# Optimization experiments

Measured on AMD Instinct MI355X. Metric: run time of the kernel, lower is better.

## Reference

```python
import jax, jax.numpy as jnp
import numpy as np

B = 128; NMAX = 128; H = 1024; HH = 256; NZ = 64; M = 20; LAT = 128; NCLS = 10; SD = 5
IN_DIM = SD + NCLS + LAT  # 143


def setup_inputs() -> dict:
    key = jax.random.key(0)
    ks = jax.random.split(key, 24)
    r = lambda i, shape, s=0.05: jax.random.normal(ks[i], shape, dtype=jnp.float32) * s
    cls_idx = jax.random.randint(ks[20], (B,), 0, NCLS)
    return dict(
        z=jax.random.normal(ks[0], (B, LAT), dtype=jnp.float32),
        classifier=jax.nn.one_hot(cls_idx, NCLS, dtype=jnp.float32),
        fc_in_W=r(1, (2 * H + 2 * HH, LAT)),
        fc_in_b=jnp.zeros((2 * H + 2 * HH,), jnp.float32),
        Wx=r(2, (4 * H, IN_DIM)),
        Wh=r(3, (4 * H, H)),
        b0=jnp.zeros((4, H), jnp.float32),
        hWx=r(4, (4 * HH, IN_DIM + H)),
        hWh=r(5, (4 * HH, HH)),
        hb=jnp.zeros((4 * HH,), jnp.float32),
        Whz_x=r(6, (4 * NZ, HH)),
        Whz_h=r(7, (4 * NZ, HH)),
        Whz_b=r(8, (4 * NZ, HH)),
        Wdz_x=r(9, (4, H, NZ), 0.1),
        Wdz_h=r(10, (4, H, NZ), 0.1),
        Wdz_b=r(11, (4, H, NZ), 0.1),
        proj_W=r(12, (6 * M + 3, H)),
        proj_b=jnp.zeros((6 * M + 3,), jnp.float32),
        eps=jax.random.normal(ks[13], (NMAX, B, 2), dtype=jnp.float32),
        umix=jax.random.uniform(ks[14], (NMAX, B, M), dtype=jnp.float32),
        upen=jax.random.uniform(ks[15], (NMAX, B, 3), dtype=jnp.float32),
    )


def _gumbel(u):
    u = jnp.clip(u, 1e-7, 1.0 - 1e-7)
    return -jnp.log(-jnp.log(u))


def reference(z, classifier, fc_in_W, fc_in_b, Wx, Wh, b0, hWx, hWh, hb,
              Whz_x, Whz_h, Whz_b, Wdz_x, Wdz_h, Wdz_b, proj_W, proj_b,
              eps, umix, upen):
    sig = jax.nn.sigmoid
    # initial states: tanh(fc_in(z)) split into h, c, h_hat, c_hat
    s = jnp.tanh(z @ fc_in_W.T + fc_in_b)
    h0 = s[:, :H]; c0 = s[:, H:2 * H]
    hh0 = s[:, 2 * H:2 * H + HH]; ch0 = s[:, 2 * H + HH:]
    prev0 = jnp.tile(jnp.array([0., 0., 1., 0., 0.], jnp.float32), (B, 1))
    empty = jnp.array([0., 0., 0., 0., 1.], jnp.float32)

    def mod(hh, Whz, Wdz):
        zg = (hh @ Whz.T).reshape(B, 4, NZ)          # hyper embedding per gate
        return jnp.einsum('bkz,khz->bkh', zg, Wdz)   # [B,4,H] gate scalings

    def step(carry, xs):
        prev, h, c, hh, ch = carry
        eps_t, um_t, up_t = xs
        x = jnp.concatenate([prev, classifier, z], axis=1)    # [B, IN_DIM]
        # hyper LSTM step on [x, h]
        hx = jnp.concatenate([x, h], axis=1)
        g4 = hx @ hWx.T + hh @ hWh.T + hb                     # [B, 4*HH]
        hi, hf, hg, ho = jnp.split(g4, 4, axis=1)
        ch_n = sig(hf) * ch + sig(hi) * jnp.tanh(hg)
        hh_n = sig(ho) * jnp.tanh(ch_n)
        # main LSTM gates modulated by hyper outputs
        dX = mod(hh_n, Whz_x, Wdz_x)
        dH = mod(hh_n, Whz_h, Wdz_h)
        dB = mod(hh_n, Whz_b, Wdz_b)
        gx = (x @ Wx.T).reshape(B, 4, H)
        gh = (h @ Wh.T).reshape(B, 4, H)
        pre = dX * gx + dH * gh + dB + b0                     # [B,4,H]
        i_, f_, g_, o_ = pre[:, 0], pre[:, 1], pre[:, 2], pre[:, 3]
        c_n = sig(f_) * c + sig(i_) * jnp.tanh(g_)
        h_n = sig(o_) * jnp.tanh(c_n)
        # MDN params + sampling
        y = h_n @ proj_W.T + proj_b                           # [B, 6M+3]
        pi_h = y[:, :M]
        mux = y[:, M:2 * M]; muy = y[:, 2 * M:3 * M]
        sxh = y[:, 3 * M:4 * M]; syh = y[:, 4 * M:5 * M]
        rhoh = y[:, 5 * M:6 * M]; pen = y[:, 6 * M:]
        k = jnp.argmax(jax.nn.log_softmax(pi_h) + _gumbel(um_t), axis=1)
        take = lambda a: jnp.take_along_axis(a, k[:, None], axis=1)[:, 0]
        mx, my = take(mux), take(muy)
        sx, sy = jnp.exp(take(sxh)), jnp.exp(take(syh))
        rho = jnp.tanh(take(rhoh))
        dx_s = mx + sx * eps_t[:, 0]
        dy_s = my + sy * (rho * eps_t[:, 0] + jnp.sqrt(1.0 - rho ** 2) * eps_t[:, 1])
        pidx = jnp.argmax(jax.nn.log_softmax(pen) + _gumbel(up_t), axis=1)
        pen_oh = jax.nn.one_hot(pidx, 3, dtype=y.dtype)
        stroke = jnp.concatenate([dx_s[:, None], dy_s[:, None], pen_oh], axis=1)
        done = pen_oh[:, 2:3] > 0.5                           # p3==1 -> empty stroke
        stroke = jnp.where(done, empty, stroke)
        return (stroke, h_n, c_n, hh_n, ch_n), stroke

    _, strokes = jax.lax.scan(jax.checkpoint(step), (prev0, h0, c0, hh0, ch0),
                              (eps, umix, upen))
    return strokes  # [NMAX, B, 5]
```

## Files before the change

kernel.cpp:

```cpp
#include <hip/hip_runtime.h>
#include <hip/hip_cooperative_groups.h>

namespace cg = cooperative_groups;

#define NBLK 256
#define NTHR 512

constexpr int WS_H    = 0;
constexpr int WS_HHS  = 131072;
constexpr int WS_Y    = 163840;
constexpr int WS_WEFF = 180224;
constexpr int WS_BAR  = WS_WEFF + 256*12288;

__device__ __forceinline__ float dot4(float4 a, float4 b){
  return a.x*b.x + a.y*b.y + a.z*b.z + a.w*b.w;
}
__device__ __forceinline__ float sigf(float x){ return 1.0f/(1.0f + expf(-x)); }
__device__ __forceinline__ float gumb(float u){
  u = fminf(fmaxf(u, 1e-7f), 1.0f - 1e-7f);
  return -logf(-logf(u));
}

__device__ __forceinline__ void st_cg(float* p, float v){
  asm volatile("global_store_dword %0, %1, off sc0 sc1" :: "v"(p), "v"(v) : "memory");
}

__device__ __forceinline__ void gridbar(unsigned* barc, unsigned n){
  asm volatile("s_waitcnt vmcnt(0)" ::: "memory");
  __syncthreads();
  if (threadIdx.x == 0){
    const unsigned g = blockIdx.x >> 4;
    unsigned old = __hip_atomic_fetch_add(barc + 32 + g*32, 1u,
                     __ATOMIC_RELAXED, __HIP_MEMORY_SCOPE_AGENT);
    if (old + 1 == n*16)
      __hip_atomic_fetch_add(barc, 1u, __ATOMIC_RELAXED, __HIP_MEMORY_SCOPE_AGENT);
    if ((blockIdx.x & 15) == 0){
      while (__hip_atomic_load(barc, __ATOMIC_RELAXED, __HIP_MEMORY_SCOPE_AGENT) < n*16)
        __builtin_amdgcn_s_sleep(1);
      __hip_atomic_store(barc + 544 + g*32, n, __ATOMIC_RELAXED, __HIP_MEMORY_SCOPE_AGENT);
    } else {
      while (__hip_atomic_load(barc + 544 + g*32, __ATOMIC_RELAXED, __HIP_MEMORY_SCOPE_AGENT) < n)
        __builtin_amdgcn_s_sleep(1);
    }
  }
  __syncthreads();
  __builtin_amdgcn_fence(__ATOMIC_ACQUIRE, "agent");
}

extern "C" __global__ void __launch_bounds__(NTHR, 1)
vae_kernel(const float* __restrict__ z,     const float* __restrict__ cls,
           const float* __restrict__ fcW,   const float* __restrict__ fcb,
           const float* __restrict__ Wx,    const float* __restrict__ Wh,
           const float* __restrict__ bias0, const float* __restrict__ hWx,
           const float* __restrict__ hWh,   const float* __restrict__ hb,
           const float* __restrict__ Whz_x, const float* __restrict__ Whz_h,
           const float* __restrict__ Whz_b, const float* __restrict__ Wdz_x,
           const float* __restrict__ Wdz_h, const float* __restrict__ Wdz_b,
           const float* __restrict__ projW, const float* __restrict__ projb,
           const float* __restrict__ eps_,  const float* __restrict__ umix,
           const float* __restrict__ upen,
           float* __restrict__ out, float* __restrict__ ws)
{
  cg::grid_group grid = cg::this_grid();
  const int tid = threadIdx.x;
  const int bid = blockIdx.x;
  const int l = tid & 63;
  const int w = tid >> 6;
  const int rq = w & 3;
  const int bh = w >> 2;

  float* hws   = ws + WS_H;
  float* hhws  = ws + WS_HHS;
  float* yws   = ws + WS_Y;
  float* weffw = ws + WS_WEFF;
  unsigned* barc = (unsigned*)(ws + WS_BAR);

  __shared__ __align__(16) float lds_h[16896];
  __shared__ __align__(16) float lds_GH[2176];
  __shared__ __align__(16) float lds_Gp[640];
  __shared__ __align__(16) float lds_prev[1152];
  __shared__ __align__(16) float lds_hWxs[4096];
  __shared__ __align__(16) float lds_hWhs[1024];
  __shared__ __align__(16) float lds_pj[1024];
  __shared__ __align__(16) float lds_cgx[2048];
  __shared__ __align__(16) float lds_cg4[512];
  __shared__ float lds_wxp[80];
  __shared__ float lds_hwxp[20];
  __shared__ float lds_b0[16];

  if (bid == 0 && tid < 33){
    unsigned* p = (tid == 0) ? barc
                : (tid < 17) ? (barc + 32 + (tid-1)*32)
                             : (barc + 544 + (tid-17)*32);
    __hip_atomic_store(p, 0u, __ATOMIC_RELAXED, __HIP_MEMORY_SCOPE_AGENT);
  }

  const bool isproj = (bid >= 128 && bid < 251);
  const int prow = bid - 128;
  float pjb = 0.f;
  if (isproj) pjb = projb[prow];

  for (int i = tid; i < 4096; i += NTHR){
    int gi = i >> 10, c = i & 1023;
    lds_hWxs[i] = hWx[(size_t)(gi*256 + bid)*1167 + 143 + c];
  }
  for (int i = tid; i < 1024; i += NTHR){
    int gi = i >> 8, c = i & 255;
    lds_hWhs[i] = hWh[(((size_t)(gi*256 + bid)) << 8) + c];
  }
  if (isproj)
    for (int i = tid; i < 1024; i += NTHR)
      lds_pj[i] = projW[((size_t)prow << 10) + i];

  const int eb = tid >> 2, ej = tid & 3;
  #pragma unroll
  for (int k = 0; k < 4; ++k){
    const float* wr = Wx + (size_t)(k*1024 + bid*4 + ej)*143;
    float a = 0.f;
    for (int n = 0; n < 10; ++n) a += cls[eb*10+n]*wr[5+n];
    const float* zr = z + (eb << 7);
    #pragma unroll 8
    for (int i = 0; i < 128; ++i) a += zr[i]*wr[15+i];
    lds_cgx[tid*4+k] = a;
  }
  float cst;
  {
    int col = 1024 + bid*4 + ej;
    float a = fcb[col];
    const float* wr = fcW + (col << 7);
    const float* zr = z + (eb << 7);
    #pragma unroll 8
    for (int i = 0; i < 128; ++i) a += zr[i]*wr[i];
    cst = tanhf(a);
  }
  {
    int col = bid*4 + ej;
    float a = fcb[col];
    const float* wr = fcW + (col << 7);
    const float* zr = z + (eb << 7);
    #pragma unroll 8
    for (int i = 0; i < 128; ++i) a += zr[i]*wr[i];
    st_cg(&hws[(eb << 10) + col], tanhf(a));
  }
  float chst = 0.f;
  if (tid < 128){
    int b = tid;
    const float* zr = z + (b << 7);
    #pragma unroll
    for (int gi = 0; gi < 4; ++gi){
      int row = gi*256 + bid;
      const float* wr = hWx + (size_t)row*1167;
      float a = hb[row];
      for (int n = 0; n < 10; ++n) a += cls[b*10+n]*wr[5+n];
      #pragma unroll 8
      for (int i = 0; i < 128; ++i) a += zr[i]*wr[15+i];
      lds_cg4[b*4+gi] = a;
    }
    {
      int col = 2304 + bid;
      float a = fcb[col];
      const float* wr = fcW + (col << 7);
      #pragma unroll 8
      for (int i = 0; i < 128; ++i) a += zr[i]*wr[i];
      chst = tanhf(a);
    }
    {
      int col = 2048 + bid;
      float a = fcb[col];
      const float* wr = fcW + (col << 7);
      #pragma unroll 8
      for (int i = 0; i < 128; ++i) a += zr[i]*wr[i];
      st_cg(&hhws[(b << 8) + bid], tanhf(a));
    }
    lds_prev[tid*9+0] = 0.f; lds_prev[tid*9+1] = 0.f; lds_prev[tid*9+2] = 1.f;
    lds_prev[tid*9+3] = 0.f; lds_prev[tid*9+4] = 0.f;
  }
  if (tid < 80){
    int r16 = tid/5, p = tid - r16*5;
    lds_wxp[tid] = Wx[(size_t)((r16>>2)*1024 + bid*4 + (r16&3))*143 + p];
  }
  if (tid < 20){
    int gi = tid/5, p = tid - gi*5;
    lds_hwxp[tid] = hWx[(size_t)(gi*256 + bid)*1167 + p];
  }
  if (tid < 16) lds_b0[tid] = bias0[(tid>>2)*1024 + bid*4 + (tid&3)];

  {
    const float* Wdzp[3] = {Wdz_x, Wdz_h, Wdz_b};
    const float* Whzp[3] = {Whz_x, Whz_h, Whz_b};
    for (int n = 0; n < 24; ++n){
      int gidx = tid + 512*n;
      int m = gidx >> 12, rem = gidx & 4095;
      int r = rem >> 8, c = rem & 255;
      int k = r >> 2, j = r & 3;
      const float* wd = Wdzp[m] + (size_t)(k*1024 + bid*4 + j)*64;
      const float* wzb = Whzp[m] + c;
      float a = 0.f;
      #pragma unroll 8
      for (int zz = 0; zz < 64; ++zz) a += wd[zz]*wzb[(k*64+zz) << 8];
      weffw[(size_t)bid*12288 + gidx] = a;
    }
  }
  grid.sync();

  unsigned barno = 0;

  const float4* wx4  = (const float4*)lds_hWxs + (rq << 8);
  const float4* whh4 = (const float4*)lds_hWhs + (rq << 6);
  const float4* pj4  = (const float4*)lds_pj;

  for (int t = 0; t <= 128; ++t){
    {
      float4 wWh[4][4];
      #pragma unroll
      for (int j = 0; j < 4; ++j){
        const int row = rq*1024 + bid*4 + j;
        #pragma unroll
        for (int m = 0; m < 4; ++m)
          wWh[j][m] = *((const float4*)(Wh + ((size_t)row << 10) + m*256) + l);
      }

      auto p1c = [&](float4 a0, float4 a1, float4 a2, float4 a3, float4 hv, int b){
        float acc[4];
        #pragma unroll
        for (int j = 0; j < 4; ++j)
          acc[j] = dot4(a0,wWh[j][0]) + dot4(a1,wWh[j][1])
                 + dot4(a2,wWh[j][2]) + dot4(a3,wWh[j][3]);
        float gac = dot4(a0, wx4[l]) + dot4(a1, wx4[64+l]) + dot4(a2, wx4[128+l])
                  + dot4(a3, wx4[192+l]) + dot4(hv, whh4[l]);
        const bool b5 = (l & 32), b4_ = (l & 16), b3 = (l & 8);
        #pragma unroll
        for (int q = 0; q < 2; ++q){
          float snd = b5 ? acc[q] : acc[q+2];
          float rcv = __shfl_xor(snd, 32, 64);
          acc[q] = (b5 ? acc[q+2] : acc[q]) + rcv;
        }
        gac += __shfl_xor(gac, 32, 64);
        {
          float snd = b4_ ? acc[0] : acc[1];
          float rcv = __shfl_xor(snd, 16, 64);
          acc[0] = (b4_ ? acc[1] : acc[0]) + rcv;
        }
        gac += __shfl_xor(gac, 16, 64);
        {
          float snd = b3 ? acc[0] : gac;
          float rcv = __shfl_xor(snd, 8, 64);
          float s = (b3 ? gac : acc[0]) + rcv;
          s += __shfl_xor(s, 4, 64);
          s += __shfl_xor(s, 2, 64);
          s += __shfl_xor(s, 1, 64);
          if ((l & 15) == 0)
            lds_GH[b*17 + rq*4 + (b5 ? 2 : 0) + (b4_ ? 1 : 0)] = s;
          else if (l == 8)
            lds_Gp[b*5 + rq] = s;
        }
        if (isproj && ((b & 3) == rq)){
          float ya = dot4(a0,pj4[l]) + dot4(a1,pj4[64+l]) + dot4(a2,pj4[128+l])
                   + dot4(a3,pj4[192+l]);
          ya += __shfl_xor(ya, 32, 64);
          ya += __shfl_xor(ya, 16, 64);
          ya += __shfl_xor(ya, 8, 64);
          ya += __shfl_xor(ya, 4, 64);
          ya += __shfl_xor(ya, 2, 64);
          ya += __shfl_xor(ya, 1, 64);
          if (l == 0) st_cg(&yws[(b << 7) + prow], ya + pjb);
        }
      };

      const float4* hb4  = (const float4*)hws;
      const float4* hhb4 = (const float4*)hhws;
      const int bq = bh*64;
      float4 A0,A1,A2,A3,AH, B0,B1,B2,B3,BH;
      {
        const float4* hp = hb4 + ((size_t)bq << 8);
        A0 = hp[l]; A1 = hp[64+l]; A2 = hp[128+l]; A3 = hp[192+l];
        AH = hhb4[(bq << 6) + l];
        const float4* hp2 = hb4 + ((size_t)(bq+1) << 8);
        B0 = hp2[l]; B1 = hp2[64+l]; B2 = hp2[128+l]; B3 = hp2[192+l];
        BH = hhb4[((bq+1) << 6) + l];
      }
      for (int it = 0; it < 64; it += 2){
        p1c(A0,A1,A2,A3,AH, bq+it);
        if (it < 62){
          const float4* hp = hb4 + ((size_t)(bq+it+2) << 8);
          A0 = hp[l]; A1 = hp[64+l]; A2 = hp[128+l]; A3 = hp[192+l];
          AH = hhb4[((bq+it+2) << 6) + l];
        }
        p1c(B0,B1,B2,B3,BH, bq+it+1);
        if (it < 62){
          const float4* hp = hb4 + ((size_t)(bq+it+3) << 8);
          B0 = hp[l]; B1 = hp[64+l]; B2 = hp[128+l]; B3 = hp[192+l];
          BH = hhb4[((bq+it+3) << 6) + l];
        }
      }
    }
    gridbar(barc, ++barno);

    float4 wf[12];
    #pragma unroll
    for (int m = 0; m < 3; ++m)
      #pragma unroll
      for (int j = 0; j < 4; ++j)
        wf[m*4+j] = *((const float4*)(weffw + (size_t)bid*12288 + m*4096 + ((rq*4+j) << 8)) + l);

    if (t >= 1){
      {
        const float4* ysrc = (const float4*)yws;
        float4 q4[8];
        #pragma unroll
        for (int k = 0; k < 8; ++k) q4[k] = ysrc[(tid>>2)*32 + (tid&3)*8 + k];
        float4* dst = (float4*)(lds_h + (tid>>2)*132 + (tid&3)*32);
        #pragma unroll
        for (int k = 0; k < 8; ++k) dst[k] = q4[k];
      }
      const int sb = tid >> 2, sq = tid & 3;
      float gm[5];
      #pragma unroll
      for (int i = 0; i < 5; ++i) gm[i] = gumb(umix[((t-1)*128 + sb)*20 + sq*5 + i]);
      const float gpe = (sq < 3) ? gumb(upen[((t-1)*128 + sb)*3 + sq]) : -1e30f;
      const float e0 = eps_[((t-1)*128 + sb)*2 + 0];
      const float e1 = eps_[((t-1)*128 + sb)*2 + 1];
      __syncthreads();
      const float* yb = lds_h + sb*132;
      float best = -1e30f; int km = 0;
      #pragma unroll
      for (int i = 0; i < 5; ++i){
        float v = yb[sq*5+i] + gm[i];
        if (v > best){ best = v; km = sq*5+i; }
      }
      #pragma unroll
      for (int d = 1; d <= 2; d <<= 1){
        float ov = __shfl_xor(best, d, 64);
        int   oi = __shfl_xor(km,   d, 64);
        if (ov > best || (ov == best && oi < km)){ best = ov; km = oi; }
      }
      float pbv = (sq < 3) ? yb[120+sq] + gpe : -1e30f;
      int pbi = sq;
      #pragma unroll
      for (int d = 1; d <= 2; d <<= 1){
        float ov = __shfl_xor(pbv, d, 64);
        int   oi = __shfl_xor(pbi, d, 64);
        if (ov > pbv || (ov == pbv && oi < pbi)){ pbv = ov; pbi = oi; }
      }
      if (sq == 0){
        const float mx = yb[20+km], my = yb[40+km];
        const float sx = expf(yb[60+km]), sy = expf(yb[80+km]);
        const float rho = tanhf(yb[100+km]);
        const float dxs = mx + sx*e0;
        const float dys = my + sy*(rho*e0 + sqrtf(1.0f - rho*rho)*e1);
        float s0,s1,s2,s3,s4;
        if (pbi == 2){ s0=0.f; s1=0.f; s2=0.f; s3=0.f; s4=1.f; }
        else { s0=dxs; s1=dys; s2=(pbi==0)?1.f:0.f; s3=(pbi==1)?1.f:0.f; s4=0.f; }
        if (bid == 0){
          float* o = out + ((t-1)*128 + sb)*5;
          st_cg(o+0, s0); st_cg(o+1, s1); st_cg(o+2, s2); st_cg(o+3, s3); st_cg(o+4, s4);
        }
        lds_prev[sb*9+0]=s0; lds_prev[sb*9+1]=s1; lds_prev[sb*9+2]=s2;
        lds_prev[sb*9+3]=s3; lds_prev[sb*9+4]=s4;
      }
      __syncthreads();
    }
    if (t == 128) break;
    if (tid < 128){
      const int b = tid;
      const float pv0 = lds_prev[b*9+0], pv1 = lds_prev[b*9+1], pv2 = lds_prev[b*9+2],
                  pv3 = lds_prev[b*9+3], pv4 = lds_prev[b*9+4];
      const float4 c4 = ((const float4*)lds_cg4)[b];
      const float cg4f[4] = {c4.x, c4.y, c4.z, c4.w};
      float gv[4];
      #pragma unroll
      for (int gi = 0; gi < 4; ++gi)
        gv[gi] = lds_Gp[b*5 + gi] + cg4f[gi]
               + pv0*lds_hwxp[gi*5+0] + pv1*lds_hwxp[gi*5+1] + pv2*lds_hwxp[gi*5+2]
               + pv3*lds_hwxp[gi*5+3] + pv4*lds_hwxp[gi*5+4];
      const float chn = sigf(gv[1])*chst + sigf(gv[0])*tanhf(gv[2]);
      chst = chn;
      const float hhn = sigf(gv[3])*tanhf(chn);
      st_cg(&hhws[(b << 8) + bid], hhn);
    }
    gridbar(barc, ++barno);

    {
      float* lds_scr = lds_h;
      const float4* hq = (const float4*)hhws;
      const int b0 = bh*64;
      float4 pf[4];
      #pragma unroll
      for (int i = 0; i < 4; ++i) pf[i] = hq[(b0 + i)*64 + l];
      #pragma unroll 4
      for (int it = 0; it < 64; ++it){
        const float4 ch = pf[it & 3];
        if (it < 60) pf[it & 3] = hq[(b0 + it + 4)*64 + l];
        const int b = b0 + it;
        float v[12];
        #pragma unroll
        for (int q = 0; q < 12; ++q) v[q] = dot4(ch, wf[q]);
        {
          const bool b5 = (l & 32), b4_ = (l & 16), b3 = (l & 8);
          #pragma unroll
          for (int q = 0; q < 6; ++q){
            float snd = b5 ? v[q] : v[q+6];
            float rcv = __shfl_xor(snd, 32, 64);
            v[q] = (b5 ? v[q+6] : v[q]) + rcv;
          }
          #pragma unroll
          for (int q = 0; q < 3; ++q){
            float snd = b4_ ? v[q] : v[q+3];
            float rcv = __shfl_xor(snd, 16, 64);
            v[q] = (b4_ ? v[q+3] : v[q]) + rcv;
          }
          float snd = b3 ? v[0] : v[1];
          float rcv = __shfl_xor(snd, 8, 64);
          float ab = (b3 ? v[1] : v[0]) + rcv;
          ab += __shfl_xor(ab, 4, 64);
          ab += __shfl_xor(ab, 2, 64);
          ab += __shfl_xor(ab, 1, 64);
          float c2 = v[2];
          c2 += __shfl_xor(c2, 8, 64);
          c2 += __shfl_xor(c2, 4, 64);
          c2 += __shfl_xor(c2, 2, 64);
          c2 += __shfl_xor(c2, 1, 64);
          const int base = (b5 ? 6 : 0) + (b4_ ? 3 : 0);
          if ((l & 15) == 0){
            lds_scr[b*50 + rq*12 + base + 0] = ab;
            lds_scr[b*50 + rq*12 + base + 2] = c2;
          } else if ((l & 15) == 8){
            lds_scr[b*50 + rq*12 + base + 1] = ab;
          }
        }
      }
      __syncthreads();
      {
        float pv[5];
        #pragma unroll
        for (int p = 0; p < 5; ++p) pv[p] = lds_prev[eb*9 + p];
        const float4 cg = ((const float4*)lds_cgx)[tid];
        const float cgxf[4] = {cg.x, cg.y, cg.z, cg.w};
        float pre[4];
        #pragma unroll
        for (int k = 0; k < 4; ++k){
          const float dXv = lds_scr[eb*50 + k*12 + ej];
          const float dHv = lds_scr[eb*50 + k*12 + 4 + ej];
          const float dBv = lds_scr[eb*50 + k*12 + 8 + ej];
          float gxv = cgxf[k];
          #pragma unroll
          for (int p = 0; p < 5; ++p) gxv += pv[p]*lds_wxp[(k*4+ej)*5 + p];
          pre[k] = dXv*gxv + dHv*lds_GH[eb*17 + k*4 + ej] + dBv + lds_b0[k*4+ej];
        }
        const float cn = sigf(pre[1])*cst + sigf(pre[0])*tanhf(pre[2]);
        cst = cn;
        const float hn = sigf(pre[3])*tanhf(cn);
        st_cg(&hws[(eb << 10) + bid*4 + ej], hn);
      }
    }
    gridbar(barc, ++barno);
  }
}

extern "C" void kernel_launch(void* const* d_in, const int* in_sizes, int n_in,
                              void* d_out, int out_size, void* d_ws, size_t ws_size,
                              hipStream_t stream)
{
  const float* z     = (const float*)d_in[0];
  const float* cls   = (const float*)d_in[1];
  const float* fcW   = (const float*)d_in[2];
  const float* fcb   = (const float*)d_in[3];
  const float* Wx    = (const float*)d_in[4];
  const float* Wh    = (const float*)d_in[5];
  const float* bias0 = (const float*)d_in[6];
  const float* hWx   = (const float*)d_in[7];
  const float* hWh   = (const float*)d_in[8];
  const float* hb    = (const float*)d_in[9];
  const float* Whz_x = (const float*)d_in[10];
  const float* Whz_h = (const float*)d_in[11];
  const float* Whz_b = (const float*)d_in[12];
  const float* Wdz_x = (const float*)d_in[13];
  const float* Wdz_h = (const float*)d_in[14];
  const float* Wdz_b = (const float*)d_in[15];
  const float* projW = (const float*)d_in[16];
  const float* projb = (const float*)d_in[17];
  const float* eps_  = (const float*)d_in[18];
  const float* umix  = (const float*)d_in[19];
  const float* upen  = (const float*)d_in[20];
  float* out = (float*)d_out;
  float* ws  = (float*)d_ws;

  void* args[] = { (void*)&z, (void*)&cls, (void*)&fcW, (void*)&fcb, (void*)&Wx, (void*)&Wh,
                   (void*)&bias0, (void*)&hWx, (void*)&hWh, (void*)&hb,
                   (void*)&Whz_x, (void*)&Whz_h, (void*)&Whz_b,
                   (void*)&Wdz_x, (void*)&Wdz_h, (void*)&Wdz_b,
                   (void*)&projW, (void*)&projb, (void*)&eps_, (void*)&umix, (void*)&upen,
                   (void*)&out, (void*)&ws };
  (void)hipLaunchCooperativeKernel((const void*)vae_kernel, dim3(NBLK), dim3(NTHR), args, 0, stream);
}
```

Measured before the change: 17.60 ms.

## Split grid barriers into arrive/wait events and overlap loads with barrier waits

Replaces each monolithic grid barrier with separate arrive and wait phases on per-event counters. Independent global loads (weff weights, gumbel noise and eps inputs, the next step's Wh register tile) are issued between arrive and wait, so they overlap with barrier latency. Barrier counters are spread onto separate lines per event. The cost is more barrier state and more register pressure from holding the Wh tile across the loop.

```diff
diff --git a/kernel.cpp b/kernel.cpp
--- a/kernel.cpp
+++ b/kernel.cpp
@@ -25,21 +25,26 @@
   asm volatile("global_store_dword %0, %1, off sc0 sc1" :: "v"(p), "v"(v) : "memory");
 }
 
-__device__ __forceinline__ void gridbar(unsigned* barc, unsigned n){
+__device__ __forceinline__ void arrive(unsigned* barc, int e, unsigned n){
   asm volatile("s_waitcnt vmcnt(0)" ::: "memory");
   __syncthreads();
   if (threadIdx.x == 0){
     const unsigned g = blockIdx.x >> 4;
-    unsigned old = __hip_atomic_fetch_add(barc + 32 + g*32, 1u,
+    unsigned old = __hip_atomic_fetch_add(barc + 96 + (e*16+g)*8, 1u,
                      __ATOMIC_RELAXED, __HIP_MEMORY_SCOPE_AGENT);
     if (old + 1 == n*16)
-      __hip_atomic_fetch_add(barc, 1u, __ATOMIC_RELAXED, __HIP_MEMORY_SCOPE_AGENT);
+      __hip_atomic_fetch_add(barc + e*32, 1u, __ATOMIC_RELAXED, __HIP_MEMORY_SCOPE_AGENT);
+  }
+}
+__device__ __forceinline__ void waitev(unsigned* barc, int e, unsigned n){
+  if (threadIdx.x == 0){
+    const unsigned g = blockIdx.x >> 4;
     if ((blockIdx.x & 15) == 0){
-      while (__hip_atomic_load(barc, __ATOMIC_RELAXED, __HIP_MEMORY_SCOPE_AGENT) < n*16)
+      while (__hip_atomic_load(barc + e*32, __ATOMIC_RELAXED, __HIP_MEMORY_SCOPE_AGENT) < n*16)
         __builtin_amdgcn_s_sleep(1);
-      __hip_atomic_store(barc + 544 + g*32, n, __ATOMIC_RELAXED, __HIP_MEMORY_SCOPE_AGENT);
+      __hip_atomic_store(barc + 512 + (e*16+g)*8, n, __ATOMIC_RELAXED, __HIP_MEMORY_SCOPE_AGENT);
     } else {
-      while (__hip_atomic_load(barc + 544 + g*32, __ATOMIC_RELAXED, __HIP_MEMORY_SCOPE_AGENT) < n)
+      while (__hip_atomic_load(barc + 512 + (e*16+g)*8, __ATOMIC_RELAXED, __HIP_MEMORY_SCOPE_AGENT) < n)
         __builtin_amdgcn_s_sleep(1);
     }
   }
@@ -88,11 +93,11 @@
   __shared__ float lds_hwxp[20];
   __shared__ float lds_b0[16];
 
-  if (bid == 0 && tid < 33){
-    unsigned* p = (tid == 0) ? barc
-                : (tid < 17) ? (barc + 32 + (tid-1)*32)
-                             : (barc + 544 + (tid-17)*32);
-    __hip_atomic_store(p, 0u, __ATOMIC_RELAXED, __HIP_MEMORY_SCOPE_AGENT);
+  if (bid == 0 && tid < 99){
+    unsigned* pc = (tid < 3)  ? (barc + tid*32)
+                 : (tid < 51) ? (barc + 96  + (tid-3)*8)
+                              : (barc + 512 + (tid-51)*8);
+    __hip_atomic_store(pc, 0u, __ATOMIC_RELAXED, __HIP_MEMORY_SCOPE_AGENT);
   }
 
   const bool isproj = (bid >= 128 && bid < 251);
@@ -203,70 +208,70 @@
   }
   grid.sync();
 
-  unsigned barno = 0;
-
   const float4* wx4  = (const float4*)lds_hWxs + (rq << 8);
   const float4* whh4 = (const float4*)lds_hWhs + (rq << 6);
   const float4* pj4  = (const float4*)lds_pj;
 
+  float4 wWh[4][4];
+  #pragma unroll
+  for (int j = 0; j < 4; ++j){
+    const int row = rq*1024 + bid*4 + j;
+    #pragma unroll
+    for (int m = 0; m < 4; ++m)
+      wWh[j][m] = *((const float4*)(Wh + ((size_t)row << 10) + m*256) + l);
+  }
+
+  auto p1c = [&](float4 a0, float4 a1, float4 a2, float4 a3, float4 hv, int b){
+    float acc[4];
+    #pragma unroll
+    for (int j = 0; j < 4; ++j)
+      acc[j] = dot4(a0,wWh[j][0]) + dot4(a1,wWh[j][1])
+             + dot4(a2,wWh[j][2]) + dot4(a3,wWh[j][3]);
+    float gac = dot4(a0, wx4[l]) + dot4(a1, wx4[64+l]) + dot4(a2, wx4[128+l])
+              + dot4(a3, wx4[192+l]) + dot4(hv, whh4[l]);
+    const bool b5 = (l & 32), b4_ = (l & 16), b3 = (l & 8);
+    #pragma unroll
+    for (int q = 0; q < 2; ++q){
+      float snd = b5 ? acc[q] : acc[q+2];
+      float rcv = __shfl_xor(snd, 32, 64);
+      acc[q] = (b5 ? acc[q+2] : acc[q]) + rcv;
+    }
+    gac += __shfl_xor(gac, 32, 64);
+    {
+      float snd = b4_ ? acc[0] : acc[1];
+      float rcv = __shfl_xor(snd, 16, 64);
+      acc[0] = (b4_ ? acc[1] : acc[0]) + rcv;
+    }
+    gac += __shfl_xor(gac, 16, 64);
+    {
+      float snd = b3 ? acc[0] : gac;
+      float rcv = __shfl_xor(snd, 8, 64);
+      float s = (b3 ? gac : acc[0]) + rcv;
+      s += __shfl_xor(s, 4, 64);
+      s += __shfl_xor(s, 2, 64);
+      s += __shfl_xor(s, 1, 64);
+      if ((l & 15) == 0)
+        lds_GH[b*17 + rq*4 + (b5 ? 2 : 0) + (b4_ ? 1 : 0)] = s;
+      else if (l == 8)
+        lds_Gp[b*5 + rq] = s;
+    }
+    if (isproj && ((b & 3) == rq)){
+      float ya = dot4(a0,pj4[l]) + dot4(a1,pj4[64+l]) + dot4(a2,pj4[128+l])
+               + dot4(a3,pj4[192+l]);
+      ya += __shfl_xor(ya, 32, 64);
+      ya += __shfl_xor(ya, 16, 64);
+      ya += __shfl_xor(ya, 8, 64);
+      ya += __shfl_xor(ya, 4, 64);
+      ya += __shfl_xor(ya, 2, 64);
+      ya += __shfl_xor(ya, 1, 64);
+      if (l == 0) st_cg(&yws[(b << 7) + prow], ya + pjb);
+    }
+  };
+
   for (int t = 0; t <= 128; ++t){
+    if (t) waitev(barc, 2, t);
+
     {
-      float4 wWh[4][4];
-      #pragma unroll
-      for (int j = 0; j < 4; ++j){
-        const int row = rq*1024 + bid*4 + j;
-        #pragma unroll
-        for (int m = 0; m < 4; ++m)
-          wWh[j][m] = *((const float4*)(Wh + ((size_t)row << 10) + m*256) + l);
-      }
-
-      auto p1c = [&](float4 a0, float4 a1, float4 a2, float4 a3, float4 hv, int b){
-        float acc[4];
-        #pragma unroll
-        for (int j = 0; j < 4; ++j)
-          acc[j] = dot4(a0,wWh[j][0]) + dot4(a1,wWh[j][1])
-                 + dot4(a2,wWh[j][2]) + dot4(a3,wWh[j][3]);
-        float gac = dot4(a0, wx4[l]) + dot4(a1, wx4[64+l]) + dot4(a2, wx4[128+l])
-                  + dot4(a3, wx4[192+l]) + dot4(hv, whh4[l]);
-        const bool b5 = (l & 32), b4_ = (l & 16), b3 = (l & 8);
-        #pragma unroll
-        for (int q = 0; q < 2; ++q){
-          float snd = b5 ? acc[q] : acc[q+2];
-          float rcv = __shfl_xor(snd, 32, 64);
-          acc[q] = (b5 ? acc[q+2] : acc[q]) + rcv;
-        }
-        gac += __shfl_xor(gac, 32, 64);
-        {
-          float snd = b4_ ? acc[0] : acc[1];
-          float rcv = __shfl_xor(snd, 16, 64);
-          acc[0] = (b4_ ? acc[1] : acc[0]) + rcv;
-        }
-        gac += __shfl_xor(gac, 16, 64);
-        {
-          float snd = b3 ? acc[0] : gac;
-          float rcv = __shfl_xor(snd, 8, 64);
-          float s = (b3 ? gac : acc[0]) + rcv;
-          s += __shfl_xor(s, 4, 64);
-          s += __shfl_xor(s, 2, 64);
-          s += __shfl_xor(s, 1, 64);
-          if ((l & 15) == 0)
-            lds_GH[b*17 + rq*4 + (b5 ? 2 : 0) + (b4_ ? 1 : 0)] = s;
-          else if (l == 8)
-            lds_Gp[b*5 + rq] = s;
-        }
-        if (isproj && ((b & 3) == rq)){
-          float ya = dot4(a0,pj4[l]) + dot4(a1,pj4[64+l]) + dot4(a2,pj4[128+l])
-                   + dot4(a3,pj4[192+l]);
-          ya += __shfl_xor(ya, 32, 64);
-          ya += __shfl_xor(ya, 16, 64);
-          ya += __shfl_xor(ya, 8, 64);
-          ya += __shfl_xor(ya, 4, 64);
-          ya += __shfl_xor(ya, 2, 64);
-          ya += __shfl_xor(ya, 1, 64);
-          if (l == 0) st_cg(&yws[(b << 7) + prow], ya + pjb);
-        }
-      };
-
       const float4* hb4  = (const float4*)hws;
       const float4* hhb4 = (const float4*)hhws;
       const int bq = bh*64;
@@ -294,7 +299,7 @@
         }
       }
     }
-    gridbar(barc, ++barno);
+    arrive(barc, 0, t+1);
 
     float4 wf[12];
     #pragma unroll
@@ -302,6 +307,16 @@
       #pragma unroll
       for (int j = 0; j < 4; ++j)
         wf[m*4+j] = *((const float4*)(weffw + (size_t)bid*12288 + m*4096 + ((rq*4+j) << 8)) + l);
+    const int sb = tid >> 2, sq = tid & 3;
+    float gm[5]; float gpe = -1e30f, e0 = 0.f, e1 = 0.f;
+    if (t >= 1){
+      #pragma unroll
+      for (int i = 0; i < 5; ++i) gm[i] = gumb(umix[((t-1)*128 + sb)*20 + sq*5 + i]);
+      if (sq < 3) gpe = gumb(upen[((t-1)*128 + sb)*3 + sq]);
+      e0 = eps_[((t-1)*128 + sb)*2 + 0];
+      e1 = eps_[((t-1)*128 + sb)*2 + 1];
+    }
+    waitev(barc, 0, t+1);
 
     if (t >= 1){
       {
@@ -313,13 +328,6 @@
         #pragma unroll
         for (int k = 0; k < 8; ++k) dst[k] = q4[k];
       }
-      const int sb = tid >> 2, sq = tid & 3;
-      float gm[5];
-      #pragma unroll
-      for (int i = 0; i < 5; ++i) gm[i] = gumb(umix[((t-1)*128 + sb)*20 + sq*5 + i]);
-      const float gpe = (sq < 3) ? gumb(upen[((t-1)*128 + sb)*3 + sq]) : -1e30f;
-      const float e0 = eps_[((t-1)*128 + sb)*2 + 0];
-      const float e1 = eps_[((t-1)*128 + sb)*2 + 1];
       __syncthreads();
       const float* yb = lds_h + sb*132;
       float best = -1e30f; int km = 0;
@@ -378,7 +386,8 @@
       const float hhn = sigf(gv[3])*tanhf(chn);
       st_cg(&hhws[(b << 8) + bid], hhn);
     }
-    gridbar(barc, ++barno);
+    arrive(barc, 1, t+1);
+    waitev(barc, 1, t+1);
 
     {
       float* lds_scr = lds_h;
@@ -453,7 +462,15 @@
         st_cg(&hws[(eb << 10) + bid*4 + ej], hn);
       }
     }
-    gridbar(barc, ++barno);
+    arrive(barc, 2, t+1);
+
+    #pragma unroll
+    for (int j = 0; j < 4; ++j){
+      const int row = rq*1024 + bid*4 + j;
+      #pragma unroll
+      for (int m = 0; m < 4; ++m)
+        wWh[j][m] = *((const float4*)(Wh + ((size_t)row << 10) + m*256) + l);
+    }
   }
 }
 
```

After: 18.08 ms. +2.8%, slower.

## Stage shared h vectors through double-buffered LDS instead of per-wave global loads

Applied to the files above, without the earlier changes.

Phase-1 h and hyper-h rows used to be loaded from global memory by every wave, each wave prefetching its own batch rows into registers. Now all waves load a shared set of four batch rows cooperatively, three float4 per lane, into one of two LDS slots, and the next set is prefetched while the current one is consumed. Each wave then reads its two rows from LDS. This cuts redundant global and L2 traffic, at the cost of a __syncthreads per iteration and extra LDS traffic.

```diff
diff --git a/kernel.cpp b/kernel.cpp
--- a/kernel.cpp
+++ b/kernel.cpp
@@ -89,10 +89,10 @@
   __shared__ float lds_b0[16];
 
   if (bid == 0 && tid < 33){
-    unsigned* p = (tid == 0) ? barc
-                : (tid < 17) ? (barc + 32 + (tid-1)*32)
-                             : (barc + 544 + (tid-17)*32);
-    __hip_atomic_store(p, 0u, __ATOMIC_RELAXED, __HIP_MEMORY_SCOPE_AGENT);
+    unsigned* pc = (tid == 0) ? barc
+                 : (tid < 17) ? (barc + 32 + (tid-1)*32)
+                              : (barc + 544 + (tid-17)*32);
+    __hip_atomic_store(pc, 0u, __ATOMIC_RELAXED, __HIP_MEMORY_SCOPE_AGENT);
   }
 
   const bool isproj = (bid >= 128 && bid < 251);
@@ -267,31 +267,46 @@
         }
       };
 
-      const float4* hb4  = (const float4*)hws;
-      const float4* hhb4 = (const float4*)hhws;
-      const int bq = bh*64;
-      float4 A0,A1,A2,A3,AH, B0,B1,B2,B3,BH;
-      {
-        const float4* hp = hb4 + ((size_t)bq << 8);
-        A0 = hp[l]; A1 = hp[64+l]; A2 = hp[128+l]; A3 = hp[192+l];
-        AH = hhb4[(bq << 6) + l];
-        const float4* hp2 = hb4 + ((size_t)(bq+1) << 8);
-        B0 = hp2[l]; B1 = hp2[64+l]; B2 = hp2[128+l]; B3 = hp2[192+l];
-        BH = hhb4[((bq+1) << 6) + l];
-      }
-      for (int it = 0; it < 64; it += 2){
-        p1c(A0,A1,A2,A3,AH, bq+it);
-        if (it < 62){
-          const float4* hp = hb4 + ((size_t)(bq+it+2) << 8);
-          A0 = hp[l]; A1 = hp[64+l]; A2 = hp[128+l]; A3 = hp[192+l];
-          AH = hhb4[((bq+it+2) << 6) + l];
-        }
-        p1c(B0,B1,B2,B3,BH, bq+it+1);
-        if (it < 62){
-          const float4* hp = hb4 + ((size_t)(bq+it+3) << 8);
-          B0 = hp[l]; B1 = hp[64+l]; B2 = hp[128+l]; B3 = hp[192+l];
-          BH = hhb4[((bq+it+3) << 6) + l];
-        }
+      float4 rr[3];
+      int doff[3];
+      auto issue = [&](int i){
+        #pragma unroll
+        for (int k = 0; k < 3; ++k){
+          const int c = w + 8*k;
+          const int q = (c < 16) ? (c >> 2) : ((c - 16) & 3);
+          const int b = (q < 2) ? (2*i + q) : (62 + 2*i + q);
+          const float* src = (c < 16)
+            ? hws + ((size_t)b << 10) + ((size_t)(c & 3) << 8)
+            : hhws + ((size_t)b << 8);
+          rr[k] = ((const float4*)src)[l];
+          doff[k] = q*1280 + ((c < 16) ? ((c & 3) << 8) : 1024);
+        }
+      };
+      auto writeslot = [&](float* slot){
+        #pragma unroll
+        for (int k = 0; k < 3; ++k)
+          ((float4*)(slot + doff[k]))[l] = rr[k];
+      };
+
+      float* slotA = lds_h;
+      float* slotB = lds_h + 5120;
+      issue(0);
+      writeslot(slotA);
+      for (int i = 0; i < 32; ++i){
+        float* cur = (i & 1) ? slotB : slotA;
+        float* nxt = (i & 1) ? slotA : slotB;
+        __syncthreads();
+        if (i < 31) issue(i+1);
+        #pragma unroll
+        for (int u = 0; u < 2; ++u){
+          const int q = bh*2 + u;
+          const int b = bh ? (64 + 2*i + u) : (2*i + u);
+          const float4* hp = (const float4*)(cur + q*1280);
+          const float4 a0 = hp[l], a1 = hp[64+l], a2 = hp[128+l], a3 = hp[192+l];
+          const float4 hv = ((const float4*)(cur + q*1280 + 1024))[l];
+          p1c(a0,a1,a2,a3,hv, b);
+        }
+        if (i < 31) writeslot(nxt);
       }
     }
     gridbar(barc, ++barno);
```

New measurement: 18.91 ms. +7.5%, slower.
